# Kernel tuning notes

Hardware: AMD Instinct MI355X
Metric: run time of the kernel (lower is better)

## Reference

```python
import jax, jax.numpy as jnp
import numpy as np

NUM_EMBED = 1024
NUM_HEADS = 16
BLOCK_SIZE = 2048


def setup_inputs() -> dict:
    key = jax.random.key(0)
    k1, k2, k3, k4, k5 = jax.random.split(key, 5)
    C = NUM_EMBED
    s = 1.0 / np.sqrt(C)
    x = jax.random.normal(k1, (2, BLOCK_SIZE, C), dtype=jnp.float32)
    # nn.Linear params: weight (out,in), bias (out,)
    w_attn = jax.random.uniform(k2, (3 * C, C), minval=-s, maxval=s, dtype=jnp.float32)
    b_attn = jax.random.uniform(k3, (3 * C,), minval=-s, maxval=s, dtype=jnp.float32)
    w_proj = jax.random.uniform(k4, (C, C), minval=-s, maxval=s, dtype=jnp.float32)
    b_proj = jax.random.uniform(k5, (C,), minval=-s, maxval=s, dtype=jnp.float32)
    return {"x": x, "w_attn": w_attn, "b_attn": b_attn, "w_proj": w_proj, "b_proj": b_proj}


def reference(x, w_attn, b_attn, w_proj, b_proj):
    B, T, C = x.shape
    H = NUM_HEADS
    D = C // H
    kqv = jnp.einsum('btc,oc->bto', x, w_attn) + b_attn  # (B,T,3C)
    # Original code splits as K, Q, V in that order.
    K, Q, V = jnp.split(kqv, 3, axis=2)
    K = K.reshape(B, T, H, D).transpose(0, 2, 1, 3)  # (B,H,T,D)
    Q = Q.reshape(B, T, H, D).transpose(0, 2, 1, 3)
    V = V.reshape(B, T, H, D).transpose(0, 2, 1, 3)
    aff = jnp.einsum('bhqd,bhkd->bhqk', Q, K) * (D ** -0.5)  # (B,H,T,T)
    causal = jnp.tril(jnp.ones((T, T), dtype=bool))
    aff = jnp.where(causal[None, None], aff, jnp.float32(-jnp.inf))
    wei = jax.nn.softmax(aff, axis=-1)
    attn = jnp.einsum('bhqk,bhkd->bhqd', wei, V)
    attn = attn.transpose(0, 2, 1, 3).reshape(B, T, C)
    out = jnp.einsum('btc,oc->bto', attn, w_proj) + b_proj
    return out
```

## Files before the change

kernel.cpp:

```cpp
#include <hip/hip_runtime.h>
#include <hip/hip_bf16.h>
#include <cstdint>

typedef __attribute__((ext_vector_type(8))) short bf16x8;
typedef __attribute__((ext_vector_type(4))) float f32x4;
typedef __attribute__((ext_vector_type(4))) uint16_t u16x4;

__device__ __forceinline__ uint16_t f2b(float f) {
  union { float f; uint32_t i; } v; v.f = f;
  return (uint16_t)((v.i + 0x7FFFu + ((v.i >> 16) & 1u)) >> 16);
}

#define GLDS16(g, l) __builtin_amdgcn_global_load_lds( \
    (const __attribute__((address_space(1))) void*)(g), \
    (__attribute__((address_space(3))) void*)(l), 16, 0, 0)

__global__ __launch_bounds__(256) void cvt_all(
    const float* __restrict__ x, const float* __restrict__ wa, const float* __restrict__ wp,
    uint16_t* __restrict__ xb, uint16_t* __restrict__ wab, uint16_t* __restrict__ wpb) {
  const int i = (blockIdx.x * 256 + threadIdx.x) * 4;
  const float* src; uint16_t* dst; int off;
  if (i < 4194304)      { src = x;  dst = xb;  off = i; }
  else if (i < 7340032) { src = wa; dst = wab; off = i - 4194304; }
  else                  { src = wp; dst = wpb; off = i - 7340032; }
  const float4 v = *(const float4*)(src + off);
  u16x4 o;
  o.x = f2b(v.x); o.y = f2b(v.y); o.z = f2b(v.z); o.w = f2b(v.w);
  *(u16x4*)(dst + off) = o;
}

template <int BM, bool OUT_BF16>
__global__ __launch_bounds__(256) void gemm_bt_bias(
    const uint16_t* __restrict__ A, const uint16_t* __restrict__ B,
    const float* __restrict__ bias, void* __restrict__ Cv,
    int M, int N, int K) {
  constexpr int MI = BM / 32;
  constexpr int CHA = BM / 16;
  constexpr int CPW = (CHA + 8) / 4;
  constexpr size_t ST_BYTES = (size_t)(BM + 128) * 32 * 2;
  constexpr size_t CT_BYTES = OUT_BF16 ? (size_t)4 * (BM / 2) * 72 * 2
                                       : (size_t)4 * (BM / 2) * 68 * 4;
  constexpr size_t LB = CT_BYTES > ST_BYTES ? CT_BYTES : ST_BYTES;
  __shared__ alignas(16) unsigned char ldsb[LB];
  uint16_t* lds = (uint16_t*)ldsb;
  const int offB = BM * 32;

  const int tid = threadIdx.x;
  const int wave = tid >> 6, lane = tid & 63;
  const int q4 = lane >> 4, l16 = lane & 15;
  const int wm = wave >> 1, wn = wave & 1;
  const long blockM = (long)blockIdx.y * BM;
  const long blockN = (long)blockIdx.x * 128;

  f32x4 acc[MI][4] = {};

  for (int k0 = 0; k0 < K; k0 += 32) {
#pragma unroll
    for (int c = 0; c < CPW; ++c) {
      const int id = c * 4 + wave;
      const bool isB = id >= CHA;
      const int a = isB ? id - CHA : id;
      const uint16_t* mat = isB ? B : A;
      const long rowBase = isB ? blockN : blockM;
      const int off = isB ? offB : 0;
      const int flat = a * 64 + lane;
      const int row = flat >> 2, seg = flat & 3;
      GLDS16(mat + (rowBase + row) * (long)K + k0 + seg * 8, lds + off + a * 512);
    }
    __syncthreads();
    bf16x8 af[MI], bfr[4];
#pragma unroll
    for (int i = 0; i < MI; ++i)
      af[i] = *(const bf16x8*)&lds[(wm * (BM / 2) + i * 16 + l16) * 32 + q4 * 8];
#pragma unroll
    for (int j = 0; j < 4; ++j)
      bfr[j] = *(const bf16x8*)&lds[offB + (wn * 64 + j * 16 + l16) * 32 + q4 * 8];
#pragma unroll
    for (int i = 0; i < MI; ++i)
#pragma unroll
      for (int j = 0; j < 4; ++j)
        acc[i][j] = __builtin_amdgcn_mfma_f32_16x16x32_bf16(af[i], bfr[j], acc[i][j], 0, 0, 0);
    __syncthreads();
  }

  if (OUT_BF16) {
    uint16_t* ct = lds + wave * (BM / 2) * 72;
#pragma unroll
    for (int j = 0; j < 4; ++j) {
      const float bv = bias[blockN + wn * 64 + j * 16 + l16];
#pragma unroll
      for (int i = 0; i < MI; ++i)
#pragma unroll
        for (int r = 0; r < 4; ++r)
          ct[(i * 16 + q4 * 4 + r) * 72 + j * 16 + l16] = f2b(acc[i][j][r] + bv);
    }
    __syncthreads();
    uint16_t* Cb = (uint16_t*)Cv;
#pragma unroll
    for (int st = 0; st < BM / 16; ++st) {
      const int flat = st * 64 + lane;
      const int row = flat >> 3, seg = flat & 7;
      const bf16x8 v = *(const bf16x8*)&ct[row * 72 + seg * 8];
      *(bf16x8*)&Cb[(blockM + wm * (BM / 2) + row) * (long)N + blockN + wn * 64 + seg * 8] = v;
    }
  } else {
    float* ct = (float*)ldsb + wave * (BM / 2) * 68;
#pragma unroll
    for (int j = 0; j < 4; ++j) {
      const float bv = bias[blockN + wn * 64 + j * 16 + l16];
#pragma unroll
      for (int i = 0; i < MI; ++i)
#pragma unroll
        for (int r = 0; r < 4; ++r)
          ct[(i * 16 + q4 * 4 + r) * 68 + j * 16 + l16] = acc[i][j][r] + bv;
    }
    __syncthreads();
    float* Cb = (float*)Cv;
#pragma unroll
    for (int st = 0; st < BM / 8; ++st) {
      const int flat = st * 64 + lane;
      const int row = flat >> 4, seg = flat & 15;
      const f32x4 v = *(const f32x4*)&ct[row * 68 + seg * 4];
      *(f32x4*)&Cb[(blockM + wm * (BM / 2) + row) * (long)N + blockN + wn * 64 + seg * 4] = v;
    }
  }
}

__global__ __launch_bounds__(256, 2) void attn_flash(
    const uint16_t* __restrict__ kqv, uint16_t* __restrict__ attn) {
  constexpr int T = 2048, C = 1024, C3 = 3072;
  __shared__ alignas(16) uint16_t Vt[2][64 * 136];
  __shared__ alignas(16) uint16_t Pt[2][4 * 2176];

  const int tid = threadIdx.x;
  const int wave = tid >> 6, lane = tid & 63;
  const int q4 = lane >> 4, l16 = lane & 15;
  const int p = blockIdx.x >> 5, bh = blockIdx.x & 31;
  const int b = bh >> 4, h = bh & 15;
  const size_t base = (size_t)b * T * C3;
  const int hD = h * 64;
  const float sc = 0.125f * 1.4426950408889634f;

  int cb = 0;

  for (int ss = 0; ss < 2; ++ss) {
    const int qb = ss ? p : 31 - p;
    const int nkt = (qb >> 1) + 1;
    const int qrow = qb * 64 + wave * 16 + l16;
    const bf16x8 qf0 = *(const bf16x8*)&kqv[base + (size_t)qrow * C3 + C + hD + q4 * 8];
    const bf16x8 qf1 = *(const bf16x8*)&kqv[base + (size_t)qrow * C3 + C + hD + 32 + q4 * 8];

    f32x4 o[4] = {};
    float m_i = -1e30f, l_i = 0.f;

    for (int kt = 0; kt < nkt; ++kt) {
      const int kbase = kt * 128;
      uint32_t* VtW = (uint32_t*)Vt[cb];
#pragma unroll
      for (int s2 = 0; s2 < 2; ++s2) {
        const int s = s2 * 256 + tid;
        const int rp = s >> 3, ch = s & 7;
        const size_t g = base + (size_t)(kbase + 2 * rp) * C3 + 2 * C + hD + ch * 8;
        const bf16x8 v0 = *(const bf16x8*)&kqv[g];
        const bf16x8 v1 = *(const bf16x8*)&kqv[g + C3];
        const int colw = (rp + 8 * ch) & 63;
        const uint32_t* a0 = (const uint32_t*)&v0;
        const uint32_t* a1 = (const uint32_t*)&v1;
#pragma unroll
        for (int i = 0; i < 8; ++i) {
          const uint32_t w = (i & 1)
              ? __builtin_amdgcn_perm(a1[i >> 1], a0[i >> 1], 0x07060302u)
              : __builtin_amdgcn_perm(a1[i >> 1], a0[i >> 1], 0x05040100u);
          VtW[(ch * 8 + i) * 68 + colw] = w;
        }
      }
      bf16x8 kf[8][2];
#pragma unroll
      for (int nk = 0; nk < 8; ++nk) {
        const uint16_t* kr = &kqv[base + (size_t)(kbase + nk * 16 + l16) * C3 + hD + q4 * 8];
        kf[nk][0] = *(const bf16x8*)kr;
        kf[nk][1] = *(const bf16x8*)(kr + 32);
      }
      f32x4 s[8];
#pragma unroll
      for (int nk = 0; nk < 8; ++nk) {
        f32x4 z = {};
        z = __builtin_amdgcn_mfma_f32_16x16x32_bf16(kf[nk][0], qf0, z, 0, 0, 0);
        z = __builtin_amdgcn_mfma_f32_16x16x32_bf16(kf[nk][1], qf1, z, 0, 0, 0);
        s[nk] = z;
      }
      if (kbase + 127 > qb * 64 + wave * 16) {
#pragma unroll
        for (int nk = 0; nk < 8; ++nk) {
          const int key0 = kbase + nk * 16 + q4 * 4;
#pragma unroll
          for (int r = 0; r < 4; ++r)
            s[nk][r] = (key0 + r <= qrow) ? s[nk][r] : -1e30f;
        }
      }
      float mloc = s[0][0];
#pragma unroll
      for (int nk = 0; nk < 8; ++nk)
#pragma unroll
        for (int r = 0; r < 4; ++r) mloc = fmaxf(mloc, s[nk][r]);
      mloc = fmaxf(mloc, __shfl_xor(mloc, 16, 64));
      mloc = fmaxf(mloc, __shfl_xor(mloc, 32, 64));
      const float mnew = fmaxf(m_i, mloc * sc);
      const float alpha = exp2f(m_i - mnew);
      const bool mchg = mnew > m_i;
      m_i = mnew;
      float rs = 0.f;
#pragma unroll
      for (int nk = 0; nk < 8; ++nk)
#pragma unroll
        for (int r = 0; r < 4; ++r) {
          const float pe = exp2f(fmaf(s[nk][r], sc, -mnew));
          s[nk][r] = pe;
          rs += pe;
        }
      rs += __shfl_xor(rs, 16, 64);
      rs += __shfl_xor(rs, 32, 64);
      l_i = l_i * alpha + rs;
      if (__any(mchg)) {
#pragma unroll
        for (int r = 0; r < 4; ++r) {
          const float ar = __shfl(alpha, q4 * 4 + r, 64);
#pragma unroll
          for (int d4 = 0; d4 < 4; ++d4) o[d4][r] *= ar;
        }
      }
      uint16_t* Pw = &Pt[cb][wave * 2176];
#pragma unroll
      for (int nk = 0; nk < 8; ++nk) {
        union { __hip_bfloat162 h2; uint32_t u; } c01, c23;
        c01.h2 = __float22bfloat162_rn(make_float2(s[nk][0], s[nk][1]));
        c23.h2 = __float22bfloat162_rn(make_float2(s[nk][2], s[nk][3]));
        uint2 pkw; pkw.x = c01.u; pkw.y = c23.u;
        *(uint2*)&Pw[l16 * 136 + nk * 16 + q4 * 4] = pkw;
      }
      __syncthreads();
#pragma unroll
      for (int ks = 0; ks < 4; ++ks) {
        const bf16x8 pf = *(const bf16x8*)&Pw[l16 * 136 + ks * 32 + q4 * 8];
#pragma unroll
        for (int d4 = 0; d4 < 4; ++d4) {
          const int d = d4 * 16 + l16;
          const int col = (ks * 32 + q4 * 8 + 16 * (d >> 3)) & 127;
          const bf16x8 vf = *(const bf16x8*)&Vt[cb][d * 136 + col];
          o[d4] = __builtin_amdgcn_mfma_f32_16x16x32_bf16(pf, vf, o[d4], 0, 0, 0);
        }
      }
      cb ^= 1;
    }
    const size_t obase = (size_t)b * T * C;
    const float linv = 1.0f / l_i;
#pragma unroll
    for (int r = 0; r < 4; ++r) {
      const float lr = __shfl(linv, q4 * 4 + r, 64);
      const int q = qb * 64 + wave * 16 + q4 * 4 + r;
      const size_t rowoff = obase + (size_t)q * C + hD;
#pragma unroll
      for (int d4 = 0; d4 < 4; ++d4)
        attn[rowoff + d4 * 16 + l16] = f2b(o[d4][r] * lr);
    }
  }
}

extern "C" void kernel_launch(void* const* d_in, const int* in_sizes, int n_in,
                              void* d_out, int out_size, void* d_ws, size_t ws_size,
                              hipStream_t stream) {
  const float* x      = (const float*)d_in[0];
  const float* w_attn = (const float*)d_in[1];
  const float* b_attn = (const float*)d_in[2];
  const float* w_proj = (const float*)d_in[3];
  const float* b_proj = (const float*)d_in[4];
  float* out = (float*)d_out;

  uint16_t* xb    = (uint16_t*)d_ws;
  uint16_t* wab   = xb  + (size_t)4096 * 1024;
  uint16_t* wpb   = wab + (size_t)3072 * 1024;
  uint16_t* kqv   = wpb + (size_t)1024 * 1024;
  uint16_t* attnb = kqv + (size_t)4096 * 3072;

  dim3 blk(256, 1, 1);
  hipLaunchKernelGGL(cvt_all, dim3(8192), blk, 0, stream, x, w_attn, w_proj, xb, wab, wpb);

  hipLaunchKernelGGL((gemm_bt_bias<128, true>), dim3(3072 / 128, 4096 / 128, 1), blk, 0, stream,
                     xb, wab, b_attn, (void*)kqv, 4096, 3072, 1024);
  hipLaunchKernelGGL(attn_flash, dim3(512, 1, 1), blk, 0, stream, kqv, attnb);
  hipLaunchKernelGGL((gemm_bt_bias<64, false>), dim3(1024 / 128, 4096 / 64, 1), blk, 0, stream,
                     attnb, wpb, b_proj, (void*)out, 4096, 1024, 1024);
}
```

Before: 215.7 us.

## Software-pipeline K/V register prefetch across fused two-strip attention loop

Flattens the two query-strip loops into a single 17-iteration loop (the paired strips always total 17 key tiles) and prefetches the next tile's K fragments and V rows into registers after the barrier, so global loads overlap the PV MFMAs and the next tile's softmax. Strip switching, output writes and state reset now happen inside the loop. This hides global load latency at the cost of extra live registers (pk, pv), which could hurt occupancy under launch_bounds(256,2).

Result: no change. 219.4 us (+1.7%).

```diff
diff --git a/kernel.cpp b/kernel.cpp
--- a/kernel.cpp
+++ b/kernel.cpp
@@ -138,131 +138,169 @@
   const int p = blockIdx.x >> 5, bh = blockIdx.x & 31;
   const int b = bh >> 4, h = bh & 15;
   const size_t base = (size_t)b * T * C3;
+  const size_t obase = (size_t)b * T * C;
   const int hD = h * 64;
   const float sc = 0.125f * 1.4426950408889634f;
 
-  int cb = 0;
-
-  for (int ss = 0; ss < 2; ++ss) {
-    const int qb = ss ? p : 31 - p;
-    const int nkt = (qb >> 1) + 1;
-    const int qrow = qb * 64 + wave * 16 + l16;
-    const bf16x8 qf0 = *(const bf16x8*)&kqv[base + (size_t)qrow * C3 + C + hD + q4 * 8];
-    const bf16x8 qf1 = *(const bf16x8*)&kqv[base + (size_t)qrow * C3 + C + hD + 32 + q4 * 8];
-
-    f32x4 o[4] = {};
-    float m_i = -1e30f, l_i = 0.f;
-
-    for (int kt = 0; kt < nkt; ++kt) {
-      const int kbase = kt * 128;
+  const int qb0 = 31 - p, qb1 = p;
+  const int nkt0 = (qb0 >> 1) + 1;
+  const int tr = tid >> 3, kch = tid & 7;
+
+  int qb = qb0;
+  int qrow = qb * 64 + wave * 16 + l16;
+  bf16x8 qf0 = *(const bf16x8*)&kqv[base + (size_t)qrow * C3 + C + hD + q4 * 8];
+  bf16x8 qf1 = *(const bf16x8*)&kqv[base + (size_t)qrow * C3 + C + hD + 32 + q4 * 8];
+
+  f32x4 o[4] = {};
+  float m_i = -1e30f, l_i = 0.f;
+  int cb = 0, kt = 0;
+  bool ss1 = false;
+
+  bf16x8 pk[8][2], pv[2][2];
+#pragma unroll
+  for (int nk = 0; nk < 8; ++nk) {
+    const uint16_t* kr = &kqv[base + (size_t)(nk * 16 + l16) * C3 + hD + q4 * 8];
+    pk[nk][0] = *(const bf16x8*)kr;
+    pk[nk][1] = *(const bf16x8*)(kr + 32);
+  }
+#pragma unroll
+  for (int s2 = 0; s2 < 2; ++s2) {
+    const size_t g = base + (size_t)(2 * (s2 * 32 + tr)) * C3 + 2 * C + hD + kch * 8;
+    pv[s2][0] = *(const bf16x8*)&kqv[g];
+    pv[s2][1] = *(const bf16x8*)&kqv[g + C3];
+  }
+
+  for (int t = 0; t < 17; ++t) {
+    const int kbase = kt * 128;
+    const bool lastOfStrip = !ss1 ? (kt == nkt0 - 1) : (t == 16);
+    const int knext = lastOfStrip ? 0 : kt + 1;
+
+    f32x4 s[8];
+#pragma unroll
+    for (int nk = 0; nk < 8; ++nk) {
+      f32x4 z = {};
+      z = __builtin_amdgcn_mfma_f32_16x16x32_bf16(pk[nk][0], qf0, z, 0, 0, 0);
+      z = __builtin_amdgcn_mfma_f32_16x16x32_bf16(pk[nk][1], qf1, z, 0, 0, 0);
+      s[nk] = z;
+    }
+    if (kbase + 127 > qb * 64 + wave * 16) {
+#pragma unroll
+      for (int nk = 0; nk < 8; ++nk) {
+        const int key0 = kbase + nk * 16 + q4 * 4;
+#pragma unroll
+        for (int r = 0; r < 4; ++r)
+          s[nk][r] = (key0 + r <= qrow) ? s[nk][r] : -1e30f;
+      }
+    }
+    float mloc = s[0][0];
+#pragma unroll
+    for (int nk = 0; nk < 8; ++nk)
+#pragma unroll
+      for (int r = 0; r < 4; ++r) mloc = fmaxf(mloc, s[nk][r]);
+    mloc = fmaxf(mloc, __shfl_xor(mloc, 16, 64));
+    mloc = fmaxf(mloc, __shfl_xor(mloc, 32, 64));
+    const float mnew = fmaxf(m_i, mloc * sc);
+    const float alpha = exp2f(m_i - mnew);
+    const bool mchg = mnew > m_i;
+    m_i = mnew;
+    float rs = 0.f;
+#pragma unroll
+    for (int nk = 0; nk < 8; ++nk)
+#pragma unroll
+      for (int r = 0; r < 4; ++r) {
+        const float pe = exp2f(fmaf(s[nk][r], sc, -mnew));
+        s[nk][r] = pe;
+        rs += pe;
+      }
+    rs += __shfl_xor(rs, 16, 64);
+    rs += __shfl_xor(rs, 32, 64);
+    l_i = l_i * alpha + rs;
+    if (__any(mchg)) {
+#pragma unroll
+      for (int r = 0; r < 4; ++r) {
+        const float ar = __shfl(alpha, q4 * 4 + r, 64);
+#pragma unroll
+        for (int d4 = 0; d4 < 4; ++d4) o[d4][r] *= ar;
+      }
+    }
+    {
       uint32_t* VtW = (uint32_t*)Vt[cb];
 #pragma unroll
       for (int s2 = 0; s2 < 2; ++s2) {
-        const int s = s2 * 256 + tid;
-        const int rp = s >> 3, ch = s & 7;
-        const size_t g = base + (size_t)(kbase + 2 * rp) * C3 + 2 * C + hD + ch * 8;
-        const bf16x8 v0 = *(const bf16x8*)&kqv[g];
-        const bf16x8 v1 = *(const bf16x8*)&kqv[g + C3];
-        const int colw = (rp + 8 * ch) & 63;
-        const uint32_t* a0 = (const uint32_t*)&v0;
-        const uint32_t* a1 = (const uint32_t*)&v1;
+        const int colw = ((s2 * 32 + tr) + 8 * kch) & 63;
+        const uint32_t* a0 = (const uint32_t*)&pv[s2][0];
+        const uint32_t* a1 = (const uint32_t*)&pv[s2][1];
 #pragma unroll
         for (int i = 0; i < 8; ++i) {
           const uint32_t w = (i & 1)
               ? __builtin_amdgcn_perm(a1[i >> 1], a0[i >> 1], 0x07060302u)
               : __builtin_amdgcn_perm(a1[i >> 1], a0[i >> 1], 0x05040100u);
-          VtW[(ch * 8 + i) * 68 + colw] = w;
+          VtW[(kch * 8 + i) * 68 + colw] = w;
         }
       }
-      bf16x8 kf[8][2];
+    }
+    uint16_t* Pw = &Pt[cb][wave * 2176];
+#pragma unroll
+    for (int nk = 0; nk < 8; ++nk) {
+      union { __hip_bfloat162 h2; uint32_t u; } c01, c23;
+      c01.h2 = __float22bfloat162_rn(make_float2(s[nk][0], s[nk][1]));
+      c23.h2 = __float22bfloat162_rn(make_float2(s[nk][2], s[nk][3]));
+      uint2 pkw; pkw.x = c01.u; pkw.y = c23.u;
+      *(uint2*)&Pw[l16 * 136 + nk * 16 + q4 * 4] = pkw;
+    }
+    __syncthreads();
+    if (t < 16) {
+      const int kb2 = knext * 128;
 #pragma unroll
       for (int nk = 0; nk < 8; ++nk) {
-        const uint16_t* kr = &kqv[base + (size_t)(kbase + nk * 16 + l16) * C3 + hD + q4 * 8];
-        kf[nk][0] = *(const bf16x8*)kr;
-        kf[nk][1] = *(const bf16x8*)(kr + 32);
-      }
-      f32x4 s[8];
-#pragma unroll
-      for (int nk = 0; nk < 8; ++nk) {
-        f32x4 z = {};
-        z = __builtin_amdgcn_mfma_f32_16x16x32_bf16(kf[nk][0], qf0, z, 0, 0, 0);
-        z = __builtin_amdgcn_mfma_f32_16x16x32_bf16(kf[nk][1], qf1, z, 0, 0, 0);
-        s[nk] = z;
-      }
-      if (kbase + 127 > qb * 64 + wave * 16) {
-#pragma unroll
-        for (int nk = 0; nk < 8; ++nk) {
-          const int key0 = kbase + nk * 16 + q4 * 4;
-#pragma unroll
-          for (int r = 0; r < 4; ++r)
-            s[nk][r] = (key0 + r <= qrow) ? s[nk][r] : -1e30f;
-        }
-      }
-      float mloc = s[0][0];
-#pragma unroll
-      for (int nk = 0; nk < 8; ++nk)
-#pragma unroll
-        for (int r = 0; r < 4; ++r) mloc = fmaxf(mloc, s[nk][r]);
-      mloc = fmaxf(mloc, __shfl_xor(mloc, 16, 64));
-      mloc = fmaxf(mloc, __shfl_xor(mloc, 32, 64));
-      const float mnew = fmaxf(m_i, mloc * sc);
-      const float alpha = exp2f(m_i - mnew);
-      const bool mchg = mnew > m_i;
-      m_i = mnew;
-      float rs = 0.f;
-#pragma unroll
-      for (int nk = 0; nk < 8; ++nk)
-#pragma unroll
-        for (int r = 0; r < 4; ++r) {
-          const float pe = exp2f(fmaf(s[nk][r], sc, -mnew));
-          s[nk][r] = pe;
-          rs += pe;
-        }
-      rs += __shfl_xor(rs, 16, 64);
-      rs += __shfl_xor(rs, 32, 64);
-      l_i = l_i * alpha + rs;
-      if (__any(mchg)) {
-#pragma unroll
-        for (int r = 0; r < 4; ++r) {
-          const float ar = __shfl(alpha, q4 * 4 + r, 64);
-#pragma unroll
-          for (int d4 = 0; d4 < 4; ++d4) o[d4][r] *= ar;
-        }
-      }
-      uint16_t* Pw = &Pt[cb][wave * 2176];
-#pragma unroll
-      for (int nk = 0; nk < 8; ++nk) {
-        union { __hip_bfloat162 h2; uint32_t u; } c01, c23;
-        c01.h2 = __float22bfloat162_rn(make_float2(s[nk][0], s[nk][1]));
-        c23.h2 = __float22bfloat162_rn(make_float2(s[nk][2], s[nk][3]));
-        uint2 pkw; pkw.x = c01.u; pkw.y = c23.u;
-        *(uint2*)&Pw[l16 * 136 + nk * 16 + q4 * 4] = pkw;
-      }
-      __syncthreads();
-#pragma unroll
-      for (int ks = 0; ks < 4; ++ks) {
-        const bf16x8 pf = *(const bf16x8*)&Pw[l16 * 136 + ks * 32 + q4 * 8];
-#pragma unroll
-        for (int d4 = 0; d4 < 4; ++d4) {
-          const int d = d4 * 16 + l16;
-          const int col = (ks * 32 + q4 * 8 + 16 * (d >> 3)) & 127;
-          const bf16x8 vf = *(const bf16x8*)&Vt[cb][d * 136 + col];
-          o[d4] = __builtin_amdgcn_mfma_f32_16x16x32_bf16(pf, vf, o[d4], 0, 0, 0);
-        }
-      }
-      cb ^= 1;
-    }
-    const size_t obase = (size_t)b * T * C;
-    const float linv = 1.0f / l_i;
-#pragma unroll
-    for (int r = 0; r < 4; ++r) {
-      const float lr = __shfl(linv, q4 * 4 + r, 64);
-      const int q = qb * 64 + wave * 16 + q4 * 4 + r;
-      const size_t rowoff = obase + (size_t)q * C + hD;
-#pragma unroll
-      for (int d4 = 0; d4 < 4; ++d4)
-        attn[rowoff + d4 * 16 + l16] = f2b(o[d4][r] * lr);
-    }
+        const uint16_t* kr = &kqv[base + (size_t)(kb2 + nk * 16 + l16) * C3 + hD + q4 * 8];
+        pk[nk][0] = *(const bf16x8*)kr;
+        pk[nk][1] = *(const bf16x8*)(kr + 32);
+      }
+#pragma unroll
+      for (int s2 = 0; s2 < 2; ++s2) {
+        const size_t g = base + (size_t)(kb2 + 2 * (s2 * 32 + tr)) * C3 + 2 * C + hD + kch * 8;
+        pv[s2][0] = *(const bf16x8*)&kqv[g];
+        pv[s2][1] = *(const bf16x8*)&kqv[g + C3];
+      }
+    }
+#pragma unroll
+    for (int ks = 0; ks < 4; ++ks) {
+      const bf16x8 pf = *(const bf16x8*)&Pw[l16 * 136 + ks * 32 + q4 * 8];
+#pragma unroll
+      for (int d4 = 0; d4 < 4; ++d4) {
+        const int d = d4 * 16 + l16;
+        const int col = (ks * 32 + q4 * 8 + 16 * (d >> 3)) & 127;
+        const bf16x8 vf = *(const bf16x8*)&Vt[cb][d * 136 + col];
+        o[d4] = __builtin_amdgcn_mfma_f32_16x16x32_bf16(pf, vf, o[d4], 0, 0, 0);
+      }
+    }
+    if (lastOfStrip) {
+      const float linv = 1.0f / l_i;
+#pragma unroll
+      for (int r = 0; r < 4; ++r) {
+        const float lr = __shfl(linv, q4 * 4 + r, 64);
+        const int q = qb * 64 + wave * 16 + q4 * 4 + r;
+        const size_t rowoff = obase + (size_t)q * C + hD;
+#pragma unroll
+        for (int d4 = 0; d4 < 4; ++d4)
+          attn[rowoff + d4 * 16 + l16] = f2b(o[d4][r] * lr);
+      }
+      if (!ss1) {
+        ss1 = true;
+        qb = qb1;
+        qrow = qb * 64 + wave * 16 + l16;
+        qf0 = *(const bf16x8*)&kqv[base + (size_t)qrow * C3 + C + hD + q4 * 8];
+        qf1 = *(const bf16x8*)&kqv[base + (size_t)qrow * C3 + C + hD + 32 + q4 * 8];
+#pragma unroll
+        for (int d4 = 0; d4 < 4; ++d4) o[d4] = (f32x4){0.f, 0.f, 0.f, 0.f};
+        m_i = -1e30f; l_i = 0.f;
+        kt = 0;
+      }
+    } else {
+      ++kt;
+    }
+    cb ^= 1;
   }
 }
 
```
